# Optimization experiments

Measured on AMD Instinct MI355X. Metric: run time of the kernel, lower is better.

Reference implementation:

```python
import jax, jax.numpy as jnp
import numpy as np
import math

D_EMB = 1024
N_HEADS = 16
SCALE = 0.02
B, T = 4, 2048


def _norm(x):
    # torch.std_mean default: unbiased std (ddof=1) over last dim
    m = jnp.mean(x, axis=-1, keepdims=True)
    s = jnp.std(x, axis=-1, keepdims=True, ddof=1)
    return (x - m) / (s + 1e-05)


def setup_inputs() -> dict:
    key = jax.random.key(0)
    kx, kw = jax.random.split(key)
    x = jax.random.normal(kx, (B, D_EMB, T), dtype=jnp.float32)
    qkv = jax.random.normal(kw, (3, N_HEADS, D_EMB, D_EMB // N_HEADS), dtype=jnp.float32) * SCALE
    return {"x": x, "qkv": qkv}


def reference(x, qkv):
    Bsz, D, Tlen = x.shape
    H = qkv.shape[1]
    # (3, B, H, T, d_head)
    h = jnp.einsum('bdt,nhde->nbhte', x, qkv)
    q, k, v = h[0], h[1], h[2]
    q = _norm(q)
    k = _norm(k)
    scale = math.sqrt(D // H)  # torch: sqrt(d_emb // H)
    attn = jnp.einsum('bhte,bhse->bhts', q, k) / scale  # [B,H,T,T]
    attn = jax.nn.softmax(attn, axis=-1)
    out = jnp.einsum('bhts,bhse->bhet', attn, v)  # [B,H,d_head,T]
    return out.reshape(Bsz, D, Tlen)
```

## Files before the change

### kernel.cpp

```cpp
#include <hip/hip_runtime.h>
#include <hip/hip_bf16.h>

#define B_SZ 4
#define NHEADS 16
#define T_SZ 2048
#define DE 1024
#define DH 64
#define BH (B_SZ*NHEADS)
#define SCL 0.18033688011112042f

typedef __attribute__((ext_vector_type(8))) short short8;
typedef __attribute__((ext_vector_type(4))) float float4v;
typedef __attribute__((ext_vector_type(2))) unsigned int uint2v;

__device__ __forceinline__ short f2bf(float f) {
    __hip_bfloat16 h = __float2bfloat16(f);
    return *reinterpret_cast<short*>(&h);
}
__device__ __forceinline__ unsigned int pack_bf2(float a, float b) {
    float2 f; f.x = a; f.y = b;
    __hip_bfloat162 h = __float22bfloat162_rn(f);
    return *reinterpret_cast<unsigned int*>(&h);
}
__device__ __forceinline__ float4v zero4() {
    float4v z = {0.f, 0.f, 0.f, 0.f};
    return z;
}
__device__ __forceinline__ int swz(int row, int g) {
    return row * 64 + (((g) ^ (row & 7)) << 3);
}
__device__ __forceinline__ void gl_lds16(const short* g, short* l) {
    __builtin_amdgcn_global_load_lds(
        (const __attribute__((address_space(1))) void*)g,
        (__attribute__((address_space(3))) void*)l, 16, 0, 0);
}

__global__ __launch_bounds__(256) void transpose_k(const float* __restrict__ src,
                                                   short* __restrict__ dst,
                                                   int R, int C) {
    __shared__ __align__(16) short tile[64 * 65];
    int c0 = blockIdx.x * 64, r0 = blockIdx.y * 64;
    src += (size_t)blockIdx.z * R * C;
    dst += (size_t)blockIdx.z * R * C;
    int tid = threadIdx.x;
#pragma unroll
    for (int it = 0; it < 16; ++it) {
        int idx = it * 256 + tid;
        int rr = idx >> 6, cc = idx & 63;
        tile[cc * 65 + rr] = f2bf(src[(size_t)(r0 + rr) * C + c0 + cc]);
    }
    __syncthreads();
#pragma unroll
    for (int it = 0; it < 16; ++it) {
        int idx = it * 256 + tid;
        int cc = idx >> 6, rr = idx & 63;
        dst[(size_t)(c0 + cc) * R + r0 + rr] = tile[cc * 65 + rr];
    }
}

__global__ __launch_bounds__(256, 2) void qkv_k(const short* __restrict__ XT,
                                                const short* __restrict__ WT,
                                                short* __restrict__ Qw,
                                                short* __restrict__ Kw,
                                                short* __restrict__ Vt) {
    __shared__ __align__(16) short ldsA[128 * 64];
    __shared__ __align__(16) short ldsB[256 * 64];
    int b  = blockIdx.x >> 4;
    int t0 = (blockIdx.x & 15) * 128;
    int n  = blockIdx.y >> 2;
    int h0 = (blockIdx.y & 3) * 4;
    int tid = threadIdx.x, wave = tid >> 6, lane = tid & 63;
    int l15 = lane & 15, quad = lane >> 4;
    int wr = wave >> 1, wc = wave & 1;

    const short* Arow = XT + ((size_t)b * T_SZ + t0) * DE;
    const short* Brow = WT + ((size_t)n * 1024 + h0 * 64) * DE;

    int rA = lane >> 3;
    int gl = (lane & 7) ^ rA;

    float4v acc[4][8];
#pragma unroll
    for (int mm = 0; mm < 4; ++mm)
#pragma unroll
        for (int j = 0; j < 8; ++j) acc[mm][j] = zero4();

    for (int k0 = 0; k0 < DE; k0 += 64) {
        __syncthreads();
#pragma unroll
        for (int it = 0; it < 4; ++it) {
            int rowbase = it * 32 + wave * 8;
            gl_lds16(&Arow[(size_t)(rowbase + rA) * DE + k0 + gl * 8],
                     &ldsA[(it * 256 + wave * 64) * 8]);
        }
#pragma unroll
        for (int it = 0; it < 8; ++it) {
            int rowbase = it * 32 + wave * 8;
            gl_lds16(&Brow[(size_t)(rowbase + rA) * DE + k0 + gl * 8],
                     &ldsB[(it * 256 + wave * 64) * 8]);
        }
        __syncthreads();
#pragma unroll
        for (int ks = 0; ks < 2; ++ks) {
            short8 af[4], bf[8];
#pragma unroll
            for (int mm = 0; mm < 4; ++mm)
                af[mm] = *(const short8*)&ldsA[swz(64 * wr + 16 * mm + l15, 4 * ks + quad)];
#pragma unroll
            for (int j = 0; j < 8; ++j)
                bf[j] = *(const short8*)&ldsB[swz(128 * wc + 16 * j + l15, 4 * ks + quad)];
#pragma unroll
            for (int mm = 0; mm < 4; ++mm)
#pragma unroll
                for (int j = 0; j < 8; ++j)
                    acc[mm][j] = __builtin_amdgcn_mfma_f32_16x16x32_bf16(af[mm], bf[j], acc[mm][j], 0, 0, 0);
        }
    }

#pragma unroll
    for (int mm = 0; mm < 4; ++mm) {
        int tbase = t0 + 64 * wr + 16 * mm;
#pragma unroll
        for (int jh = 0; jh < 2; ++jh) {
            int h = h0 + 2 * wc + jh;
            int bh = b * NHEADS + h;
            if (n < 2) {
                float oscale = (n == 0) ? SCL : 1.0f;
                float mu[4], inv[4];
#pragma unroll
                for (int r = 0; r < 4; ++r) {
                    float s1 = 0.f, s2 = 0.f;
#pragma unroll
                    for (int jj = 0; jj < 4; ++jj) {
                        float v = acc[mm][4 * jh + jj][r];
                        s1 += v; s2 += v * v;
                    }
                    for (int sh = 1; sh < 16; sh <<= 1) {
                        s1 += __shfl_xor(s1, sh, 64);
                        s2 += __shfl_xor(s2, sh, 64);
                    }
                    mu[r] = s1 * (1.0f / 64.0f);
                    float var = (s2 - 64.0f * mu[r] * mu[r]) * (1.0f / 63.0f);
                    var = fmaxf(var, 0.0f);
                    inv[r] = oscale / (sqrtf(var) + 1e-5f);
                }
                short* dst = (n == 0 ? Qw : Kw) + (size_t)bh * T_SZ * DH;
#pragma unroll
                for (int r = 0; r < 4; ++r) {
                    int t = tbase + quad * 4 + r;
#pragma unroll
                    for (int jj = 0; jj < 4; ++jj) {
                        float v = (acc[mm][4 * jh + jj][r] - mu[r]) * inv[r];
                        dst[(size_t)t * DH + 16 * jj + l15] = f2bf(v);
                    }
                }
            } else {
#pragma unroll
                for (int r = 0; r < 4; ++r) {
                    int t = tbase + quad * 4 + r;
#pragma unroll
                    for (int jj = 0; jj < 4; ++jj) {
                        Vt[((size_t)bh * DH + 16 * jj + l15) * T_SZ + t] =
                            f2bf(acc[mm][4 * jh + jj][r]);
                    }
                }
            }
        }
    }
}

__global__ __launch_bounds__(256, 4) void attn_k(const short* __restrict__ Qw,
                                                 const short* __restrict__ Kw,
                                                 const short* __restrict__ Vt,
                                                 float* __restrict__ out) {
    __shared__ __align__(16) char smem[34816];
    short* ldsK = (short*)smem;
    short* ldsV = (short*)(smem + 8192);
    short* ldsP = (short*)(smem + 16384);
    float* ldsO = (float*)smem;

    int bh = blockIdx.x;
    int t0 = blockIdx.y * 128;
    int b = bh >> 4, h = bh & 15;
    int tid = threadIdx.x, wave = tid >> 6, lane = tid & 63;
    int l15 = lane & 15, quad = lane >> 4;
    int tw = t0 + 32 * wave;

    const short* Qp = Qw + (size_t)bh * T_SZ * DH;
    const short* Kp = Kw + (size_t)bh * T_SZ * DH;
    const short* Vp = Vt + (size_t)bh * DH * T_SZ;
    short* Pw = ldsP + wave * 32 * 72;

    int rA = lane >> 3;
    int gl = (lane & 7) ^ rA;

    short8 qf[2][2];
#pragma unroll
    for (int tt = 0; tt < 2; ++tt)
#pragma unroll
        for (int ks = 0; ks < 2; ++ks)
            qf[tt][ks] = *(const short8*)&Qp[(size_t)(tw + 16 * tt + l15) * DH + ks * 32 + quad * 8];

    const short one_bf = (short)0x3F80;
    short8 ones = {one_bf, one_bf, one_bf, one_bf, one_bf, one_bf, one_bf, one_bf};

    float4v o[2][4];
    float4v ol[2];
#pragma unroll
    for (int tt = 0; tt < 2; ++tt) {
        ol[tt] = zero4();
#pragma unroll
        for (int j = 0; j < 4; ++j) o[tt][j] = zero4();
    }

    for (int s0 = 0; s0 < T_SZ; s0 += 64) {
        __syncthreads();
#pragma unroll
        for (int it = 0; it < 2; ++it) {
            int rowbase = it * 32 + wave * 8;
            gl_lds16(&Kp[(size_t)(s0 + rowbase + rA) * DH + gl * 8],
                     &ldsK[(it * 256 + wave * 64) * 8]);
            gl_lds16(&Vp[(size_t)(rowbase + rA) * T_SZ + s0 + gl * 8],
                     &ldsV[(it * 256 + wave * 64) * 8]);
        }
        __syncthreads();

#pragma unroll
        for (int j = 0; j < 4; ++j) {
            short8 k0 = *(const short8*)&ldsK[swz(16 * j + l15, quad)];
            short8 k1 = *(const short8*)&ldsK[swz(16 * j + l15, 4 + quad)];
#pragma unroll
            for (int tt = 0; tt < 2; ++tt) {
                float4v z = zero4();
                z = __builtin_amdgcn_mfma_f32_16x16x32_bf16(k0, qf[tt][0], z, 0, 0, 0);
                z = __builtin_amdgcn_mfma_f32_16x16x32_bf16(k1, qf[tt][1], z, 0, 0, 0);
                float p0 = __builtin_amdgcn_exp2f(z[0]);
                float p1 = __builtin_amdgcn_exp2f(z[1]);
                float p2 = __builtin_amdgcn_exp2f(z[2]);
                float p3 = __builtin_amdgcn_exp2f(z[3]);
                uint2v u = { pack_bf2(p0, p1), pack_bf2(p2, p3) };
                *(uint2v*)&Pw[(16 * tt + l15) * 72 + 16 * j + quad * 4] = u;
            }
        }

        short8 pf[2][2];
#pragma unroll
        for (int tt = 0; tt < 2; ++tt) {
            pf[tt][0] = *(const short8*)&Pw[(16 * tt + l15) * 72 + quad * 8];
            pf[tt][1] = *(const short8*)&Pw[(16 * tt + l15) * 72 + 32 + quad * 8];
            ol[tt] = __builtin_amdgcn_mfma_f32_16x16x32_bf16(pf[tt][0], ones, ol[tt], 0, 0, 0);
            ol[tt] = __builtin_amdgcn_mfma_f32_16x16x32_bf16(pf[tt][1], ones, ol[tt], 0, 0, 0);
        }
#pragma unroll
        for (int j = 0; j < 4; ++j) {
            short8 v0 = *(const short8*)&ldsV[swz(16 * j + l15, quad)];
            short8 v1 = *(const short8*)&ldsV[swz(16 * j + l15, 4 + quad)];
#pragma unroll
            for (int tt = 0; tt < 2; ++tt) {
                o[tt][j] = __builtin_amdgcn_mfma_f32_16x16x32_bf16(pf[tt][0], v0, o[tt][j], 0, 0, 0);
                o[tt][j] = __builtin_amdgcn_mfma_f32_16x16x32_bf16(pf[tt][1], v1, o[tt][j], 0, 0, 0);
            }
        }
    }

    float4v rinv[2];
#pragma unroll
    for (int tt = 0; tt < 2; ++tt)
#pragma unroll
        for (int r = 0; r < 4; ++r)
            rinv[tt][r] = 1.0f / ol[tt][r];

#pragma unroll
    for (int ph = 0; ph < 2; ++ph) {
        __syncthreads();
        if ((wave >> 1) == ph) {
            float* Ow = ldsO + (wave & 1) * (64 * 36);
#pragma unroll
            for (int tt = 0; tt < 2; ++tt)
#pragma unroll
                for (int j = 0; j < 4; ++j) {
                    float4v ov = o[tt][j] * rinv[tt];
                    *(float4v*)&Ow[(16 * j + l15) * 36 + 16 * tt + quad * 4] = ov;
                }
        }
        __syncthreads();
#pragma unroll
        for (int it = 0; it < 4; ++it) {
            int idx = it * 256 + tid;
            int rg = idx >> 9;
            int rid = idx & 511;
            int e = rid >> 3, t4 = (rid & 7) * 4;
            *(float4v*)&out[((size_t)(b * DE + h * DH + e)) * T_SZ + t0 + 32 * (2 * ph + rg) + t4] =
                *(const float4v*)&ldsO[rg * (64 * 36) + e * 36 + t4];
        }
    }
}

extern "C" void kernel_launch(void* const* d_in, const int* in_sizes, int n_in,
                              void* d_out, int out_size, void* d_ws, size_t ws_size,
                              hipStream_t stream) {
    const float* x = (const float*)d_in[0];
    const float* w = (const float*)d_in[1];
    float* out = (float*)d_out;
    char* ws = (char*)d_ws;

    const size_t XT_BYTES = (size_t)B_SZ * T_SZ * DE * 2;
    const size_t WT_BYTES = (size_t)3 * NHEADS * DH * DE * 2;
    const size_t QKV_BYTES = (size_t)BH * T_SZ * DH * 2;

    short* XT = (short*)(ws);
    short* WT = (short*)(ws + XT_BYTES);
    short* Qw = (short*)(ws + XT_BYTES + WT_BYTES);
    short* Kw = (short*)(ws + XT_BYTES + WT_BYTES + QKV_BYTES);
    short* Vt = (short*)(ws + XT_BYTES + WT_BYTES + 2 * QKV_BYTES);

    transpose_k<<<dim3(T_SZ / 64, DE / 64, B_SZ), 256, 0, stream>>>(x, XT, DE, T_SZ);
    transpose_k<<<dim3(1, DE / 64, 3 * NHEADS), 256, 0, stream>>>(w, WT, DE, DH);
    qkv_k<<<dim3(64, 12), 256, 0, stream>>>(XT, WT, Qw, Kw, Vt);
    attn_k<<<dim3(BH, T_SZ / 128), 256, 0, stream>>>(Qw, Kw, Vt, out);
}
```

Baseline: 235.6 us.

## Double-buffer QKV GEMM LDS loads and halve the N tile to double the grid

The QKV projection kernel now uses two LDS buffers and issues the next K-slice's global-to-LDS loads while the current slice runs on MFMA, so memory latency can overlap with compute. It also shrinks the per-block N tile from 256 to 128 columns, giving 2 heads per block and 24 grid rows instead of 12. That cuts per-thread accumulators from 32 to 16 float4v and doubles block count, which improves occupancy and load balance across CUs. In exchange, each block reuses its A tile over fewer output columns, so activation tiles are re-read from memory twice as often.

```diff
diff --git a/kernel.cpp b/kernel.cpp
--- a/kernel.cpp
+++ b/kernel.cpp
@@ -63,12 +63,12 @@
                                                 short* __restrict__ Qw,
                                                 short* __restrict__ Kw,
                                                 short* __restrict__ Vt) {
-    __shared__ __align__(16) short ldsA[128 * 64];
-    __shared__ __align__(16) short ldsB[256 * 64];
+    __shared__ __align__(16) short ldsA[2][128 * 64];
+    __shared__ __align__(16) short ldsB[2][128 * 64];
     int b  = blockIdx.x >> 4;
     int t0 = (blockIdx.x & 15) * 128;
-    int n  = blockIdx.y >> 2;
-    int h0 = (blockIdx.y & 3) * 4;
+    int n  = blockIdx.y >> 3;
+    int h0 = (blockIdx.y & 7) * 2;
     int tid = threadIdx.x, wave = tid >> 6, lane = tid & 63;
     int l15 = lane & 15, quad = lane >> 4;
     int wr = wave >> 1, wc = wave & 1;
@@ -79,90 +79,95 @@
     int rA = lane >> 3;
     int gl = (lane & 7) ^ rA;
 
-    float4v acc[4][8];
+    float4v acc[4][4];
 #pragma unroll
     for (int mm = 0; mm < 4; ++mm)
 #pragma unroll
-        for (int j = 0; j < 8; ++j) acc[mm][j] = zero4();
-
-    for (int k0 = 0; k0 < DE; k0 += 64) {
-        __syncthreads();
+        for (int j = 0; j < 4; ++j) acc[mm][j] = zero4();
+
+    auto STAGE = [&](short* La, short* Lb, int k0) {
 #pragma unroll
         for (int it = 0; it < 4; ++it) {
             int rowbase = it * 32 + wave * 8;
             gl_lds16(&Arow[(size_t)(rowbase + rA) * DE + k0 + gl * 8],
-                     &ldsA[(it * 256 + wave * 64) * 8]);
-        }
-#pragma unroll
-        for (int it = 0; it < 8; ++it) {
-            int rowbase = it * 32 + wave * 8;
+                     &La[(it * 256 + wave * 64) * 8]);
             gl_lds16(&Brow[(size_t)(rowbase + rA) * DE + k0 + gl * 8],
-                     &ldsB[(it * 256 + wave * 64) * 8]);
-        }
-        __syncthreads();
+                     &Lb[(it * 256 + wave * 64) * 8]);
+        }
+    };
+    auto COMPUTE = [&](const short* La, const short* Lb) {
 #pragma unroll
         for (int ks = 0; ks < 2; ++ks) {
-            short8 af[4], bf[8];
+            short8 af[4], bf[4];
 #pragma unroll
             for (int mm = 0; mm < 4; ++mm)
-                af[mm] = *(const short8*)&ldsA[swz(64 * wr + 16 * mm + l15, 4 * ks + quad)];
-#pragma unroll
-            for (int j = 0; j < 8; ++j)
-                bf[j] = *(const short8*)&ldsB[swz(128 * wc + 16 * j + l15, 4 * ks + quad)];
+                af[mm] = *(const short8*)&La[swz(64 * wr + 16 * mm + l15, 4 * ks + quad)];
+#pragma unroll
+            for (int j = 0; j < 4; ++j)
+                bf[j] = *(const short8*)&Lb[swz(64 * wc + 16 * j + l15, 4 * ks + quad)];
 #pragma unroll
             for (int mm = 0; mm < 4; ++mm)
 #pragma unroll
-                for (int j = 0; j < 8; ++j)
+                for (int j = 0; j < 4; ++j)
                     acc[mm][j] = __builtin_amdgcn_mfma_f32_16x16x32_bf16(af[mm], bf[j], acc[mm][j], 0, 0, 0);
         }
-    }
-
+    };
+
+    STAGE(ldsA[0], ldsB[0], 0);
+    __syncthreads();
+    for (int k0 = 0; k0 < DE; k0 += 128) {
+        STAGE(ldsA[1], ldsB[1], k0 + 64);
+        COMPUTE(ldsA[0], ldsB[0]);
+        __syncthreads();
+        if (k0 + 128 < DE)
+            STAGE(ldsA[0], ldsB[0], k0 + 128);
+        COMPUTE(ldsA[1], ldsB[1]);
+        __syncthreads();
+    }
+
+    int h = h0 + wc;
+    int bh = b * NHEADS + h;
 #pragma unroll
     for (int mm = 0; mm < 4; ++mm) {
         int tbase = t0 + 64 * wr + 16 * mm;
-#pragma unroll
-        for (int jh = 0; jh < 2; ++jh) {
-            int h = h0 + 2 * wc + jh;
-            int bh = b * NHEADS + h;
-            if (n < 2) {
-                float oscale = (n == 0) ? SCL : 1.0f;
-                float mu[4], inv[4];
-#pragma unroll
-                for (int r = 0; r < 4; ++r) {
-                    float s1 = 0.f, s2 = 0.f;
-#pragma unroll
-                    for (int jj = 0; jj < 4; ++jj) {
-                        float v = acc[mm][4 * jh + jj][r];
-                        s1 += v; s2 += v * v;
-                    }
-                    for (int sh = 1; sh < 16; sh <<= 1) {
-                        s1 += __shfl_xor(s1, sh, 64);
-                        s2 += __shfl_xor(s2, sh, 64);
-                    }
-                    mu[r] = s1 * (1.0f / 64.0f);
-                    float var = (s2 - 64.0f * mu[r] * mu[r]) * (1.0f / 63.0f);
-                    var = fmaxf(var, 0.0f);
-                    inv[r] = oscale / (sqrtf(var) + 1e-5f);
-                }
-                short* dst = (n == 0 ? Qw : Kw) + (size_t)bh * T_SZ * DH;
-#pragma unroll
-                for (int r = 0; r < 4; ++r) {
-                    int t = tbase + quad * 4 + r;
-#pragma unroll
-                    for (int jj = 0; jj < 4; ++jj) {
-                        float v = (acc[mm][4 * jh + jj][r] - mu[r]) * inv[r];
-                        dst[(size_t)t * DH + 16 * jj + l15] = f2bf(v);
-                    }
-                }
-            } else {
-#pragma unroll
-                for (int r = 0; r < 4; ++r) {
-                    int t = tbase + quad * 4 + r;
-#pragma unroll
-                    for (int jj = 0; jj < 4; ++jj) {
-                        Vt[((size_t)bh * DH + 16 * jj + l15) * T_SZ + t] =
-                            f2bf(acc[mm][4 * jh + jj][r]);
-                    }
+        if (n < 2) {
+            float oscale = (n == 0) ? SCL : 1.0f;
+            float mu[4], inv[4];
+#pragma unroll
+            for (int r = 0; r < 4; ++r) {
+                float s1 = 0.f, s2 = 0.f;
+#pragma unroll
+                for (int jj = 0; jj < 4; ++jj) {
+                    float v = acc[mm][jj][r];
+                    s1 += v; s2 += v * v;
+                }
+                for (int sh = 1; sh < 16; sh <<= 1) {
+                    s1 += __shfl_xor(s1, sh, 64);
+                    s2 += __shfl_xor(s2, sh, 64);
+                }
+                mu[r] = s1 * (1.0f / 64.0f);
+                float var = (s2 - 64.0f * mu[r] * mu[r]) * (1.0f / 63.0f);
+                var = fmaxf(var, 0.0f);
+                inv[r] = oscale / (sqrtf(var) + 1e-5f);
+            }
+            short* dst = (n == 0 ? Qw : Kw) + (size_t)bh * T_SZ * DH;
+#pragma unroll
+            for (int r = 0; r < 4; ++r) {
+                int t = tbase + quad * 4 + r;
+#pragma unroll
+                for (int jj = 0; jj < 4; ++jj) {
+                    float v = (acc[mm][jj][r] - mu[r]) * inv[r];
+                    dst[(size_t)t * DH + 16 * jj + l15] = f2bf(v);
+                }
+            }
+        } else {
+#pragma unroll
+            for (int r = 0; r < 4; ++r) {
+                int t = tbase + quad * 4 + r;
+#pragma unroll
+                for (int jj = 0; jj < 4; ++jj) {
+                    Vt[((size_t)bh * DH + 16 * jj + l15) * T_SZ + t] =
+                        f2bf(acc[mm][jj][r]);
                 }
             }
         }
@@ -316,6 +321,6 @@
 
     transpose_k<<<dim3(T_SZ / 64, DE / 64, B_SZ), 256, 0, stream>>>(x, XT, DE, T_SZ);
     transpose_k<<<dim3(1, DE / 64, 3 * NHEADS), 256, 0, stream>>>(w, WT, DE, DH);
-    qkv_k<<<dim3(64, 12), 256, 0, stream>>>(XT, WT, Qw, Kw, Vt);
+    qkv_k<<<dim3(64, 24), 256, 0, stream>>>(XT, WT, Qw, Kw, Vt);
     attn_k<<<dim3(BH, T_SZ / 128), 256, 0, stream>>>(Qw, Kw, Vt, out);
 }
```

Result: no change. 240.3 us (+2.0%).
